# Performance work log

Measured on AMD Instinct MI355X. Metric: run time of the kernel, lower is better.

The kernel has to match this reference:

```python
import jax, jax.numpy as jnp
import numpy as np

N = 50000   # nodes
E = 800000  # edges (avg degree 16)
C = 128     # hidden_channels
G = 128     # graphs in batch
L0, L1 = 512, 256  # linear_hidden_channels
P = 2       # num_params (output per graph)


def setup_inputs() -> dict:
    key = jax.random.key(0)
    ks = iter(jax.random.split(key, 48))

    def w(shape):
        return jax.random.normal(next(ks), shape, jnp.float32) / np.float32(np.sqrt(shape[0]))

    inp = {}
    inp["x"] = jax.random.normal(next(ks), (N, 4), jnp.float32)
    inp["edge_index"] = jax.random.randint(next(ks), (2, E), 0, N, dtype=jnp.int32)
    inp["edge_attr"] = jax.random.normal(next(ks), (E, 3), jnp.float32)
    inp["batch"] = jnp.sort(jax.random.randint(next(ks), (N,), 0, G, dtype=jnp.int32))
    # TransformerConv params: layer 0 (in=4) and shared layer (in=C, applied twice
    # because `[GConv(...)]*(n-1)` reuses the same module object).
    for i, din in enumerate([4, C]):
        inp[f"Wq{i}"] = w((din, C)); inp[f"bq{i}"] = jnp.zeros((C,), jnp.float32)
        inp[f"Wk{i}"] = w((din, C)); inp[f"bk{i}"] = jnp.zeros((C,), jnp.float32)
        inp[f"Wv{i}"] = w((din, C)); inp[f"bv{i}"] = jnp.zeros((C,), jnp.float32)
        inp[f"We{i}"] = w((3, C))   # lin_edge has no bias
        inp[f"Ws{i}"] = w((din, C)); inp[f"bs{i}"] = jnp.zeros((C,), jnp.float32)
    inp["Wl0"] = w((C, L0));  inp["bl0"] = jnp.zeros((L0,), jnp.float32)
    inp["Wl1"] = w((L0, L1)); inp["bl1"] = jnp.zeros((L1,), jnp.float32)
    inp["Wl2"] = w((L1, P));  inp["bl2"] = jnp.zeros((P,), jnp.float32)
    return inp


def tconv(x, src, dst, e_attr, Wq, bq, Wk, bk, Wv, bv, We, Ws, bs):
    # TransformerConv (heads=1, edge_dim, root_weight=True, beta=False)
    n = x.shape[0]
    c = Wq.shape[1]
    q = x @ Wq + bq            # [N, C]
    k = x @ Wk + bk
    v = x @ Wv + bv
    e = e_attr @ We            # [E, C]
    kj = k[src] + e            # [E, C] key at source + edge emb
    vj = v[src] + e            # [E, C] value at source + edge emb
    logits = jnp.sum(q[dst] * kj, axis=-1) / jnp.sqrt(jnp.float32(c))  # [E]
    # softmax over incoming edges of each target node
    m = jax.ops.segment_max(logits, dst, num_segments=n)
    a = jnp.exp(logits - m[dst])
    denom = jax.ops.segment_sum(a, dst, num_segments=n)
    alpha = a / denom[dst]
    out = jax.ops.segment_sum(vj * alpha[:, None], dst, num_segments=n)
    return out + x @ Ws + bs   # root/skip connection


def reference(x, edge_index, edge_attr, batch,
              Wq0, bq0, Wk0, bk0, Wv0, bv0, We0, Ws0, bs0,
              Wq1, bq1, Wk1, bk1, Wv1, bv1, We1, Ws1, bs1,
              Wl0, bl0, Wl1, bl1, Wl2, bl2):
    src, dst = edge_index[0], edge_index[1]
    # layer 0
    h = tconv(x, src, dst, edge_attr, Wq0, bq0, Wk0, bk0, Wv0, bv0, We0, Ws0, bs0)
    h = jax.nn.leaky_relu(h, 0.01)  # dropout is identity in eval
    # layers 1..2 share weights (Python list-multiplication of modules)
    for _ in range(2):
        h = tconv(h, src, dst, edge_attr, Wq1, bq1, Wk1, bk1, Wv1, bv1, We1, Ws1, bs1)
        h = jax.nn.leaky_relu(h, 0.01)
    # global_add_pool
    g = jax.ops.segment_sum(h, batch, num_segments=G)  # [G, C]
    # MLP head
    g = jax.nn.relu(g @ Wl0 + bl0)
    g = jax.nn.relu(g @ Wl1 + bl1)
    g = g @ Wl2 + bl2                                  # [G, 2]
    return jnp.ravel(g)                                # [G*2]
```

## Files before the change

### kernel.cpp

```cpp
#include <hip/hip_runtime.h>
#include <math.h>

#define N_NODES 50000
#define N_EDGES 800000
#define CDIM    128
#define GDIM    128
#define L0DIM   512
#define L1DIM   256

typedef unsigned int uint;
typedef unsigned short ushort;
typedef __attribute__((ext_vector_type(8))) short short8;
typedef __attribute__((ext_vector_type(4))) float f32x4;

__device__ inline ushort f2bf(float f) {
  uint u = __float_as_uint(f);
  uint r = (u + 0x7fffu + ((u >> 16) & 1u)) >> 16;
  return (ushort)r;
}
__device__ inline float bflo(uint u) { return __uint_as_float(u << 16); }
__device__ inline float bfhi(uint u) { return __uint_as_float(u & 0xffff0000u); }

__global__ void hist_kernel(const int* __restrict__ dst, int* counts, int E) {
  int e = blockIdx.x * 256 + threadIdx.x;
  if (e < E) atomicAdd(&counts[dst[e]], 1);
}

__global__ void scan_blocks(const int* __restrict__ counts, int* excl, int* bsums, int N) {
  __shared__ int s[1024];
  int tid = threadIdx.x;
  int i = blockIdx.x * 1024 + tid;
  int v = (i < N) ? counts[i] : 0;
  s[tid] = v;
  __syncthreads();
  for (int off = 1; off < 1024; off <<= 1) {
    int t = (tid >= off) ? s[tid - off] : 0;
    __syncthreads();
    s[tid] += t;
    __syncthreads();
  }
  if (i < N) excl[i] = s[tid] - v;
  if (tid == 1023) bsums[blockIdx.x] = s[1023];
}

__global__ void scan_sums(int* bsums, int nb) {
  int lane = threadIdx.x;
  int orig = (lane < nb) ? bsums[lane] : 0;
  int v = orig;
#pragma unroll
  for (int off = 1; off < 64; off <<= 1) {
    int t = __shfl_up(v, off);
    if (lane >= off) v += t;
  }
  if (lane < nb) bsums[lane] = v - orig;
}

__global__ void scan_add(const int* __restrict__ excl, const int* __restrict__ bsums,
                         int* indptr, int N, int E) {
  int i = blockIdx.x * 1024 + threadIdx.x;
  if (i < N) indptr[i] = excl[i] + bsums[blockIdx.x];
  if (i == 0) indptr[N] = E;
}

__global__ void scatter2_kernel(const int* __restrict__ dst, const int* __restrict__ src,
                                const float* __restrict__ attr,
                                const int* __restrict__ indptr,
                                int* cursor, int* csr_src, float4* csr_attr, int E) {
  int e = blockIdx.x * 256 + threadIdx.x;
  if (e < E) {
    int d = dst[e];
    int pos = atomicAdd(&cursor[d], 1);
    int i = indptr[d] + pos;
    csr_src[i] = src[e];
    csr_attr[i] = make_float4(attr[e * 3 + 0], attr[e * 3 + 1], attr[e * 3 + 2], 0.f);
  }
}

__global__ void l0_qkvs(const float* __restrict__ x,
                        const float* __restrict__ Wq, const float* __restrict__ bq,
                        const float* __restrict__ Wk, const float* __restrict__ bk,
                        const float* __restrict__ Wv, const float* __restrict__ bv,
                        const float* __restrict__ Ws, const float* __restrict__ bs,
                        float* __restrict__ q, ushort* __restrict__ kvb,
                        float* __restrict__ hs, int N) {
  __shared__ float W[4][4][128];
  __shared__ float B[4][128];
  int tid = threadIdx.x;
  for (int i = tid; i < 4 * 128; i += 256) {
    W[0][i >> 7][i & 127] = Wq[i];
    W[1][i >> 7][i & 127] = Wk[i];
    W[2][i >> 7][i & 127] = Wv[i];
    W[3][i >> 7][i & 127] = Ws[i];
  }
  for (int i = tid; i < 128; i += 256) {
    B[0][i] = bq[i]; B[1][i] = bk[i]; B[2][i] = bv[i]; B[3][i] = bs[i];
  }
  __syncthreads();
  int gid = blockIdx.x * 256 + tid;
  int n = gid >> 7, c = gid & 127;
  if (n >= N) return;
  float x0 = x[n * 4 + 0], x1 = x[n * 4 + 1], x2 = x[n * 4 + 2], x3 = x[n * 4 + 3];
  float qv = x0 * W[0][0][c] + x1 * W[0][1][c] + x2 * W[0][2][c] + x3 * W[0][3][c] + B[0][c];
  float kv = x0 * W[1][0][c] + x1 * W[1][1][c] + x2 * W[1][2][c] + x3 * W[1][3][c] + B[1][c];
  float vv = x0 * W[2][0][c] + x1 * W[2][1][c] + x2 * W[2][2][c] + x3 * W[2][3][c] + B[2][c];
  float sv = x0 * W[3][0][c] + x1 * W[3][1][c] + x2 * W[3][2][c] + x3 * W[3][3][c] + B[3][c];
  q[n * 128 + c] = qv;
  kvb[(size_t)n * 256 + c]       = f2bf(kv);
  kvb[(size_t)n * 256 + 128 + c] = f2bf(vv);
  hs[n * 128 + c] = sv;
}

__global__ void prep_w(const float* __restrict__ Wq, const float* __restrict__ Wk,
                       const float* __restrict__ Wv, const float* __restrict__ Ws,
                       ushort* __restrict__ wt) {
  int idx = blockIdx.x * 256 + threadIdx.x;
  int z = idx >> 14, rem = idx & 16383;
  int k_ = rem >> 7, c_ = rem & 127;
  const float* W = (z == 0) ? Wq : (z == 1) ? Wk : (z == 2) ? Wv : Ws;
  wt[z * 16384 + c_ * 128 + k_] = f2bf(W[k_ * 128 + c_]);
}

#define LDA 136
#define TPB_TILES 4
__global__ __launch_bounds__(256) void gemm_mfma(
    const ushort* __restrict__ Hbf, const ushort* __restrict__ wtg,
    const float* __restrict__ bq, const float* __restrict__ bk,
    const float* __restrict__ bv, const float* __restrict__ bs,
    float* __restrict__ q, ushort* __restrict__ kvb,
    float* __restrict__ hs, int N, int nTiles) {
  int z = blockIdx.z;
  const float* bb = (z == 0) ? bq : (z == 1) ? bk : (z == 2) ? bv : bs;
  __shared__ ushort Alds[64 * LDA];
  __shared__ ushort Wlds[128 * LDA];
  int tid = threadIdx.x;

  {
    const uint* wg = (const uint*)(wtg + z * 16384);
    uint* wl = (uint*)Wlds;
    for (int i = tid; i < 8192; i += 256) {
      int c_ = i >> 6, kp = i & 63;
      wl[c_ * (LDA / 2) + kp] = wg[i];
    }
  }

  int w = tid >> 6, lane = tid & 63;
  int m_ = lane & 15, quad = lane >> 4;
  const uint* hg = (const uint*)Hbf;

  for (int tt = 0; tt < TPB_TILES; tt++) {
    int tile = blockIdx.x * TPB_TILES + tt;
    if (tile >= nTiles) break;
    int n0 = tile * 64;
    __syncthreads();
    {
      uint* al = (uint*)Alds;
      for (int i = tid; i < 4096; i += 256) {
        int r = i >> 6, kp = i & 63;
        int grow = n0 + r; grow = (grow < N) ? grow : (N - 1);
        al[r * (LDA / 2) + kp] = hg[(size_t)grow * 64 + kp];
      }
    }
    __syncthreads();

    f32x4 acc[8];
#pragma unroll
    for (int ct = 0; ct < 8; ct++) acc[ct] = 0.f;
#pragma unroll
    for (int kc = 0; kc < 4; kc++) {
      short8 af = *(const short8*)&Alds[(w * 16 + m_) * LDA + kc * 32 + quad * 8];
#pragma unroll
      for (int ct = 0; ct < 8; ct++) {
        short8 bf = *(const short8*)&Wlds[(ct * 16 + m_) * LDA + kc * 32 + quad * 8];
        acc[ct] = __builtin_amdgcn_mfma_f32_16x16x32_bf16(af, bf, acc[ct], 0, 0, 0);
      }
    }

#pragma unroll
    for (int ct = 0; ct < 8; ct++) {
      int col = ct * 16 + m_;
      float bcol = bb[col];
#pragma unroll
      for (int reg = 0; reg < 4; reg++) {
        int n = n0 + w * 16 + quad * 4 + reg;
        if (n < N) {
          float o = acc[ct][reg] + bcol;
          if (z == 0)      q[(size_t)n * 128 + col] = o;
          else if (z == 3) hs[(size_t)n * 128 + col] = o;
          else             kvb[(size_t)n * 256 + ((z == 2) ? 128 : 0) + col] = f2bf(o);
        }
      }
    }
  }
}

__global__ __launch_bounds__(256) void attn_fused(
    const float* __restrict__ q, const ushort* __restrict__ kv,
    const int* __restrict__ indptr, const int* __restrict__ csr_src,
    const float4* __restrict__ csr_attr, const float* __restrict__ We,
    float* __restrict__ h, ushort* __restrict__ hbf, int N) {
  __shared__ float WeS[384];
  int tid = threadIdx.x;
  for (int i = tid; i < 384; i += 256) WeS[i] = We[i];
  __syncthreads();
  int lane = tid & 63;
  int g = lane >> 4, gl = lane & 15;
  int c = gl * 8;
  float we0[8], we1[8], we2[8];
#pragma unroll
  for (int j = 0; j < 8; j++) {
    we0[j] = WeS[c + j]; we1[j] = WeS[128 + c + j]; we2[j] = WeS[256 + c + j];
  }
  const uint* kvw = (const uint*)kv;

  int waveId = blockIdx.x * 4 + (tid >> 6);
  int stride = gridDim.x * 4;

  for (int n = waveId; n < N; n += stride) {
    float4 qa  = *(const float4*)&q[(size_t)n * 128 + c];
    float4 qb4 = *(const float4*)&q[(size_t)n * 128 + c + 4];
    float qv[8] = {qa.x, qa.y, qa.z, qa.w, qb4.x, qb4.y, qb4.z, qb4.w};

    float t0 = 0.f, t1 = 0.f, t2 = 0.f;
#pragma unroll
    for (int j = 0; j < 8; j++) {
      t0 = fmaf(we0[j], qv[j], t0);
      t1 = fmaf(we1[j], qv[j], t1);
      t2 = fmaf(we2[j], qv[j], t2);
    }
#pragma unroll
    for (int off = 1; off < 16; off <<= 1) {
      t0 += __shfl_xor(t0, off);
      t1 += __shfl_xor(t1, off);
      t2 += __shfl_xor(t2, off);
    }

    float4 sk0 = *(const float4*)&h[(size_t)n * 128 + c];
    float4 sk1 = *(const float4*)&h[(size_t)n * 128 + c + 4];
    int beg = indptr[n], end = indptr[n + 1];

    if (end > beg) {
      float m = -3.4e38f, d = 0.f;
      float sa0 = 0.f, sa1 = 0.f, sa2 = 0.f;
      float acc[8];
#pragma unroll
      for (int j = 0; j < 8; j++) acc[j] = 0.f;

      int i = beg + g;
      int sj = 0; float4 at = make_float4(0.f, 0.f, 0.f, 0.f);
      if (i < end) { sj = csr_src[i]; at = csr_attr[i]; }
      for (; i < end; i += 4) {
        int sjc = sj; float4 atc = at;
        int inx = i + 4;
        if (inx < end) { sj = csr_src[inx]; at = csr_attr[inx]; }
        const uint4* kp = (const uint4*)(kvw + (size_t)sjc * 128);
        uint4 kr = kp[gl];
        uint4 vr = kp[16 + gl];
        float kx[8], vx[8];
        kx[0] = bflo(kr.x); kx[1] = bfhi(kr.x); kx[2] = bflo(kr.y); kx[3] = bfhi(kr.y);
        kx[4] = bflo(kr.z); kx[5] = bfhi(kr.z); kx[6] = bflo(kr.w); kx[7] = bfhi(kr.w);
        vx[0] = bflo(vr.x); vx[1] = bfhi(vr.x); vx[2] = bflo(vr.y); vx[3] = bfhi(vr.y);
        vx[4] = bflo(vr.z); vx[5] = bfhi(vr.z); vx[6] = bflo(vr.w); vx[7] = bfhi(vr.w);
        float p = 0.f;
#pragma unroll
        for (int j = 0; j < 8; j++) p = fmaf(qv[j], kx[j], p);
        p += __shfl_xor(p, 1); p += __shfl_xor(p, 2);
        p += __shfl_xor(p, 4); p += __shfl_xor(p, 8);
        p = fmaf(atc.x, t0, p);
        p = fmaf(atc.y, t1, p);
        p = fmaf(atc.z, t2, p);
        float l = p * 0.08838834764831845f;
        float nm = fmaxf(m, l);
        float sf = __expf(m - nm);
        float a = __expf(l - nm);
        d = d * sf + a;
        sa0 = sa0 * sf + a * atc.x;
        sa1 = sa1 * sf + a * atc.y;
        sa2 = sa2 * sf + a * atc.z;
#pragma unroll
        for (int j = 0; j < 8; j++) acc[j] = fmaf(acc[j], sf, a * vx[j]);
        m = nm;
      }
#pragma unroll
      for (int off = 16; off < 64; off <<= 1) {
        float m2 = __shfl_xor(m, off);
        float d2 = __shfl_xor(d, off);
        float nm = fmaxf(m, m2);
        float s1 = __expf(m - nm), s2 = __expf(m2 - nm);
        d = d * s1 + d2 * s2;
        sa0 = sa0 * s1 + __shfl_xor(sa0, off) * s2;
        sa1 = sa1 * s1 + __shfl_xor(sa1, off) * s2;
        sa2 = sa2 * s1 + __shfl_xor(sa2, off) * s2;
#pragma unroll
        for (int j = 0; j < 8; j++) {
          float a2 = __shfl_xor(acc[j], off);
          acc[j] = acc[j] * s1 + a2 * s2;
        }
        m = nm;
      }
      float inv = 1.f / d;
#pragma unroll
      for (int j = 0; j < 8; j++) {
        float ecorr = sa0 * we0[j] + sa1 * we1[j] + sa2 * we2[j];
        float o = (acc[j] + ecorr) * inv;
        if (j < 4) { (&sk0.x)[j] += o; } else { (&sk1.x)[j - 4] += o; }
      }
    }
    sk0.x = (sk0.x > 0.f) ? sk0.x : 0.01f * sk0.x;
    sk0.y = (sk0.y > 0.f) ? sk0.y : 0.01f * sk0.y;
    sk0.z = (sk0.z > 0.f) ? sk0.z : 0.01f * sk0.z;
    sk0.w = (sk0.w > 0.f) ? sk0.w : 0.01f * sk0.w;
    sk1.x = (sk1.x > 0.f) ? sk1.x : 0.01f * sk1.x;
    sk1.y = (sk1.y > 0.f) ? sk1.y : 0.01f * sk1.y;
    sk1.z = (sk1.z > 0.f) ? sk1.z : 0.01f * sk1.z;
    sk1.w = (sk1.w > 0.f) ? sk1.w : 0.01f * sk1.w;
    if (g == 0) {
      *(float4*)&h[(size_t)n * 128 + c] = sk0;
      *(float4*)&h[(size_t)n * 128 + c + 4] = sk1;
      uint4 pb;
      pb.x = (uint)f2bf(sk0.x) | ((uint)f2bf(sk0.y) << 16);
      pb.y = (uint)f2bf(sk0.z) | ((uint)f2bf(sk0.w) << 16);
      pb.z = (uint)f2bf(sk1.x) | ((uint)f2bf(sk1.y) << 16);
      pb.w = (uint)f2bf(sk1.z) | ((uint)f2bf(sk1.w) << 16);
      *(uint4*)&hbf[(size_t)n * 128 + c] = pb;
    }
  }
}

__global__ void pool_kernel(const float* __restrict__ h, const int* __restrict__ batch,
                            float* __restrict__ gout, int N) {
  int tid = threadIdx.x;
  int sub = tid >> 6;
  int c = 2 * (tid & 63);
  int n0 = blockIdx.x * 64 + sub * 16;
  if (n0 >= N) return;
  int n1 = min(n0 + 16, N);
  float a0 = 0.f, a1 = 0.f;
  int cur = batch[n0];
  for (int n = n0; n < n1; n++) {
    int b = batch[n];
    if (b != cur) {
      atomicAdd(&gout[cur * 128 + c], a0);
      atomicAdd(&gout[cur * 128 + c + 1], a1);
      a0 = 0.f; a1 = 0.f; cur = b;
    }
    float2 hv = *(const float2*)&h[(size_t)n * 128 + c];
    a0 += hv.x; a1 += hv.y;
  }
  atomicAdd(&gout[cur * 128 + c], a0);
  atomicAdd(&gout[cur * 128 + c + 1], a1);
}

__global__ __launch_bounds__(256) void mlp_fused(
    const float* __restrict__ gp,
    const float* __restrict__ Wl0, const float* __restrict__ bl0,
    const float* __restrict__ Wl1, const float* __restrict__ bl1,
    const float* __restrict__ Wl2, const float* __restrict__ bl2,
    float* __restrict__ out) {
  int g = blockIdx.x;
  int tid = threadIdx.x;
  __shared__ float xin[CDIM];
  __shared__ float h1[L0DIM];
  __shared__ float h2[L1DIM];
  __shared__ float r0s[4], r1s[4];
  if (tid < CDIM) xin[tid] = gp[g * CDIM + tid];
  __syncthreads();
  for (int c = tid; c < L0DIM; c += 256) {
    float a0 = 0.f, a1 = 0.f, a2 = 0.f, a3 = 0.f;
#pragma unroll 4
    for (int kk = 0; kk < CDIM; kk += 4) {
      a0 = fmaf(xin[kk + 0], Wl0[(kk + 0) * L0DIM + c], a0);
      a1 = fmaf(xin[kk + 1], Wl0[(kk + 1) * L0DIM + c], a1);
      a2 = fmaf(xin[kk + 2], Wl0[(kk + 2) * L0DIM + c], a2);
      a3 = fmaf(xin[kk + 3], Wl0[(kk + 3) * L0DIM + c], a3);
    }
    h1[c] = fmaxf((a0 + a1) + (a2 + a3) + bl0[c], 0.f);
  }
  __syncthreads();
  {
    int c = tid;
    float a0 = 0.f, a1 = 0.f, a2 = 0.f, a3 = 0.f;
#pragma unroll 4
    for (int kk = 0; kk < L0DIM; kk += 4) {
      a0 = fmaf(h1[kk + 0], Wl1[(kk + 0) * L1DIM + c], a0);
      a1 = fmaf(h1[kk + 1], Wl1[(kk + 1) * L1DIM + c], a1);
      a2 = fmaf(h1[kk + 2], Wl1[(kk + 2) * L1DIM + c], a2);
      a3 = fmaf(h1[kk + 3], Wl1[(kk + 3) * L1DIM + c], a3);
    }
    h2[c] = fmaxf((a0 + a1) + (a2 + a3) + bl1[c], 0.f);
  }
  __syncthreads();
  float p0 = h2[tid] * Wl2[tid * 2 + 0];
  float p1 = h2[tid] * Wl2[tid * 2 + 1];
#pragma unroll
  for (int off = 32; off > 0; off >>= 1) {
    p0 += __shfl_down(p0, off);
    p1 += __shfl_down(p1, off);
  }
  int wv = tid >> 6, ln = tid & 63;
  if (ln == 0) { r0s[wv] = p0; r1s[wv] = p1; }
  __syncthreads();
  if (tid == 0) out[g * 2 + 0] = r0s[0] + r0s[1] + r0s[2] + r0s[3] + bl2[0];
  if (tid == 1) out[g * 2 + 1] = r1s[0] + r1s[1] + r1s[2] + r1s[3] + bl2[1];
}

extern "C" void kernel_launch(void* const* d_in, const int* in_sizes, int n_in,
                              void* d_out, int out_size, void* d_ws, size_t ws_size,
                              hipStream_t stream) {
  const int N = N_NODES, E = N_EDGES;
  const float* x    = (const float*)d_in[0];
  const int*   ei   = (const int*)d_in[1];
  const float* attr = (const float*)d_in[2];
  const int*   batch= (const int*)d_in[3];
  const int* src = ei;
  const int* dst = ei + E;

  const float *Wq0 = (const float*)d_in[4],  *bq0 = (const float*)d_in[5];
  const float *Wk0 = (const float*)d_in[6],  *bk0 = (const float*)d_in[7];
  const float *Wv0 = (const float*)d_in[8],  *bv0 = (const float*)d_in[9];
  const float *We0 = (const float*)d_in[10];
  const float *Ws0 = (const float*)d_in[11], *bs0 = (const float*)d_in[12];
  const float *Wq1 = (const float*)d_in[13], *bq1 = (const float*)d_in[14];
  const float *Wk1 = (const float*)d_in[15], *bk1 = (const float*)d_in[16];
  const float *Wv1 = (const float*)d_in[17], *bv1 = (const float*)d_in[18];
  const float *We1 = (const float*)d_in[19];
  const float *Ws1 = (const float*)d_in[20], *bs1 = (const float*)d_in[21];
  const float *Wl0 = (const float*)d_in[22], *bl0 = (const float*)d_in[23];
  const float *Wl1 = (const float*)d_in[24], *bl1 = (const float*)d_in[25];
  const float *Wl2 = (const float*)d_in[26], *bl2 = (const float*)d_in[27];

  size_t off = 0;
  auto carve = [&](size_t bytes) {
    void* p = (char*)d_ws + off;
    off += (bytes + 255) & ~(size_t)255;
    return p;
  };
  float*  hA       = (float*)carve((size_t)N * CDIM * 4);
  float*  hB       = (float*)carve((size_t)N * CDIM * 4);
  float*  qb       = (float*)carve((size_t)N * CDIM * 4);
  ushort* kvb      = (ushort*)carve((size_t)N * 256 * 2);
  ushort* hbf      = (ushort*)carve((size_t)N * CDIM * 2);
  int*    indptr   = (int*)carve((size_t)(N + 1) * 4);
  int*    csr_src  = (int*)carve((size_t)E * 4);
  float4* csr_attr = (float4*)carve((size_t)E * 16);
  int*    cc       = (int*)carve((size_t)2 * N * 4);
  int*    counts   = cc;
  int*    cursor   = cc + N;
  int*    excl     = (int*)carve((size_t)N * 4);
  int*    bsums    = (int*)carve((size_t)64 * 4);
  ushort* wt1      = (ushort*)carve((size_t)4 * 16384 * 2);
  float*  gp       = (float*)carve((size_t)GDIM * CDIM * 4);

  hipMemsetAsync(cc, 0, (size_t)2 * N * 4, stream);
  hipMemsetAsync(gp, 0, (size_t)GDIM * CDIM * 4, stream);

  int nscan = (N + 1023) / 1024;
  hist_kernel<<<(E + 255) / 256, 256, 0, stream>>>(dst, counts, E);
  scan_blocks<<<nscan, 1024, 0, stream>>>(counts, excl, bsums, N);
  scan_sums<<<1, 64, 0, stream>>>(bsums, nscan);
  scan_add<<<nscan, 1024, 0, stream>>>(excl, bsums, indptr, N, E);
  scatter2_kernel<<<(E + 255) / 256, 256, 0, stream>>>(dst, src, attr, indptr, cursor,
                                                       csr_src, csr_attr, E);
  prep_w<<<256, 256, 0, stream>>>(Wq1, Wk1, Wv1, Ws1, wt1);

  int nTiles = (N + 63) / 64;
  dim3 gemmGrid((nTiles + TPB_TILES - 1) / TPB_TILES, 1, 4);
  int attnBlocks = 2048;

  l0_qkvs<<<(N * 128 + 255) / 256, 256, 0, stream>>>(
      x, Wq0, bq0, Wk0, bk0, Wv0, bv0, Ws0, bs0, qb, kvb, hA, N);
  attn_fused<<<attnBlocks, 256, 0, stream>>>(qb, kvb, indptr, csr_src, csr_attr, We0,
                                             hA, hbf, N);

  gemm_mfma<<<gemmGrid, 256, 0, stream>>>(hbf, wt1, bq1, bk1, bv1, bs1, qb, kvb, hB, N, nTiles);
  attn_fused<<<attnBlocks, 256, 0, stream>>>(qb, kvb, indptr, csr_src, csr_attr, We1,
                                             hB, hbf, N);

  gemm_mfma<<<gemmGrid, 256, 0, stream>>>(hbf, wt1, bq1, bk1, bv1, bs1, qb, kvb, hA, N, nTiles);
  attn_fused<<<attnBlocks, 256, 0, stream>>>(qb, kvb, indptr, csr_src, csr_attr, We1,
                                             hA, hbf, N);

  pool_kernel<<<(N + 63) / 64, 256, 0, stream>>>(hA, batch, gp, N);
  mlp_fused<<<GDIM, 256, 0, stream>>>(gp, Wl0, bl0, Wl1, bl1, Wl2, bl2, (float*)d_out);
}
```

Before: 620.0 us.

## Store q in bf16, launch one wave per node, fuse pooling into final attention

```diff
diff --git a/kernel.cpp b/kernel.cpp
--- a/kernel.cpp
+++ b/kernel.cpp
@@ -81,7 +81,7 @@
                         const float* __restrict__ Wk, const float* __restrict__ bk,
                         const float* __restrict__ Wv, const float* __restrict__ bv,
                         const float* __restrict__ Ws, const float* __restrict__ bs,
-                        float* __restrict__ q, ushort* __restrict__ kvb,
+                        ushort* __restrict__ qbf, ushort* __restrict__ kvb,
                         float* __restrict__ hs, int N) {
   __shared__ float W[4][4][128];
   __shared__ float B[4][128];
@@ -104,7 +104,7 @@
   float kv = x0 * W[1][0][c] + x1 * W[1][1][c] + x2 * W[1][2][c] + x3 * W[1][3][c] + B[1][c];
   float vv = x0 * W[2][0][c] + x1 * W[2][1][c] + x2 * W[2][2][c] + x3 * W[2][3][c] + B[2][c];
   float sv = x0 * W[3][0][c] + x1 * W[3][1][c] + x2 * W[3][2][c] + x3 * W[3][3][c] + B[3][c];
-  q[n * 128 + c] = qv;
+  qbf[(size_t)n * 128 + c] = f2bf(qv);
   kvb[(size_t)n * 256 + c]       = f2bf(kv);
   kvb[(size_t)n * 256 + 128 + c] = f2bf(vv);
   hs[n * 128 + c] = sv;
@@ -126,7 +126,7 @@
     const ushort* __restrict__ Hbf, const ushort* __restrict__ wtg,
     const float* __restrict__ bq, const float* __restrict__ bk,
     const float* __restrict__ bv, const float* __restrict__ bs,
-    float* __restrict__ q, ushort* __restrict__ kvb,
+    ushort* __restrict__ qbf, ushort* __restrict__ kvb,
     float* __restrict__ hs, int N, int nTiles) {
   int z = blockIdx.z;
   const float* bb = (z == 0) ? bq : (z == 1) ? bk : (z == 2) ? bv : bs;
@@ -184,7 +184,7 @@
         int n = n0 + w * 16 + quad * 4 + reg;
         if (n < N) {
           float o = acc[ct][reg] + bcol;
-          if (z == 0)      q[(size_t)n * 128 + col] = o;
+          if (z == 0)      qbf[(size_t)n * 128 + col] = f2bf(o);
           else if (z == 3) hs[(size_t)n * 128 + col] = o;
           else             kvb[(size_t)n * 256 + ((z == 2) ? 128 : 0) + col] = f2bf(o);
         }
@@ -193,16 +193,20 @@
   }
 }
 
-__global__ __launch_bounds__(256) void attn_fused(
-    const float* __restrict__ q, const ushort* __restrict__ kv,
+template <int MODE>
+__global__ __launch_bounds__(256) void attn_fused_t(
+    const ushort* __restrict__ qbf, const ushort* __restrict__ kv,
     const int* __restrict__ indptr, const int* __restrict__ csr_src,
     const float4* __restrict__ csr_attr, const float* __restrict__ We,
-    float* __restrict__ h, ushort* __restrict__ hbf, int N) {
+    float* __restrict__ h, ushort* __restrict__ hbf,
+    const int* __restrict__ batch, float* __restrict__ gp, int N) {
   __shared__ float WeS[384];
   int tid = threadIdx.x;
   for (int i = tid; i < 384; i += 256) WeS[i] = We[i];
   __syncthreads();
   int lane = tid & 63;
+  int n = blockIdx.x * 4 + (tid >> 6);
+  if (n >= N) return;
   int g = lane >> 4, gl = lane & 15;
   int c = gl * 8;
   float we0[8], we1[8], we2[8];
@@ -212,107 +216,105 @@
   }
   const uint* kvw = (const uint*)kv;
 
-  int waveId = blockIdx.x * 4 + (tid >> 6);
-  int stride = gridDim.x * 4;
-
-  for (int n = waveId; n < N; n += stride) {
-    float4 qa  = *(const float4*)&q[(size_t)n * 128 + c];
-    float4 qb4 = *(const float4*)&q[(size_t)n * 128 + c + 4];
-    float qv[8] = {qa.x, qa.y, qa.z, qa.w, qb4.x, qb4.y, qb4.z, qb4.w};
-
-    float t0 = 0.f, t1 = 0.f, t2 = 0.f;
+  uint4 qr = ((const uint4*)(qbf + (size_t)n * 128))[gl];
+  float qv[8];
+  qv[0] = bflo(qr.x); qv[1] = bfhi(qr.x); qv[2] = bflo(qr.y); qv[3] = bfhi(qr.y);
+  qv[4] = bflo(qr.z); qv[5] = bfhi(qr.z); qv[6] = bflo(qr.w); qv[7] = bfhi(qr.w);
+
+  float t0 = 0.f, t1 = 0.f, t2 = 0.f;
+#pragma unroll
+  for (int j = 0; j < 8; j++) {
+    t0 = fmaf(we0[j], qv[j], t0);
+    t1 = fmaf(we1[j], qv[j], t1);
+    t2 = fmaf(we2[j], qv[j], t2);
+  }
+#pragma unroll
+  for (int off = 1; off < 16; off <<= 1) {
+    t0 += __shfl_xor(t0, off);
+    t1 += __shfl_xor(t1, off);
+    t2 += __shfl_xor(t2, off);
+  }
+
+  float4 sk0 = *(const float4*)&h[(size_t)n * 128 + c];
+  float4 sk1 = *(const float4*)&h[(size_t)n * 128 + c + 4];
+  int beg = indptr[n], end = indptr[n + 1];
+
+  if (end > beg) {
+    float m = -3.4e38f, d = 0.f;
+    float sa0 = 0.f, sa1 = 0.f, sa2 = 0.f;
+    float acc[8];
+#pragma unroll
+    for (int j = 0; j < 8; j++) acc[j] = 0.f;
+
+    int i = beg + g;
+    int sj = 0; float4 at = make_float4(0.f, 0.f, 0.f, 0.f);
+    if (i < end) { sj = csr_src[i]; at = csr_attr[i]; }
+    for (; i < end; i += 4) {
+      int sjc = sj; float4 atc = at;
+      int inx = i + 4;
+      if (inx < end) { sj = csr_src[inx]; at = csr_attr[inx]; }
+      const uint4* kp = (const uint4*)(kvw + (size_t)sjc * 128);
+      uint4 kr = kp[gl];
+      uint4 vr = kp[16 + gl];
+      float kx[8], vx[8];
+      kx[0] = bflo(kr.x); kx[1] = bfhi(kr.x); kx[2] = bflo(kr.y); kx[3] = bfhi(kr.y);
+      kx[4] = bflo(kr.z); kx[5] = bfhi(kr.z); kx[6] = bflo(kr.w); kx[7] = bfhi(kr.w);
+      vx[0] = bflo(vr.x); vx[1] = bfhi(vr.x); vx[2] = bflo(vr.y); vx[3] = bfhi(vr.y);
+      vx[4] = bflo(vr.z); vx[5] = bfhi(vr.z); vx[6] = bflo(vr.w); vx[7] = bfhi(vr.w);
+      float p = 0.f;
+#pragma unroll
+      for (int j = 0; j < 8; j++) p = fmaf(qv[j], kx[j], p);
+      p += __shfl_xor(p, 1); p += __shfl_xor(p, 2);
+      p += __shfl_xor(p, 4); p += __shfl_xor(p, 8);
+      p = fmaf(atc.x, t0, p);
+      p = fmaf(atc.y, t1, p);
+      p = fmaf(atc.z, t2, p);
+      float l = p * 0.08838834764831845f;
+      float nm = fmaxf(m, l);
+      float sf = __expf(m - nm);
+      float a = __expf(l - nm);
+      d = d * sf + a;
+      sa0 = sa0 * sf + a * atc.x;
+      sa1 = sa1 * sf + a * atc.y;
+      sa2 = sa2 * sf + a * atc.z;
+#pragma unroll
+      for (int j = 0; j < 8; j++) acc[j] = fmaf(acc[j], sf, a * vx[j]);
+      m = nm;
+    }
+#pragma unroll
+    for (int off = 16; off < 64; off <<= 1) {
+      float m2 = __shfl_xor(m, off);
+      float d2 = __shfl_xor(d, off);
+      float nm = fmaxf(m, m2);
+      float s1 = __expf(m - nm), s2 = __expf(m2 - nm);
+      d = d * s1 + d2 * s2;
+      sa0 = sa0 * s1 + __shfl_xor(sa0, off) * s2;
+      sa1 = sa1 * s1 + __shfl_xor(sa1, off) * s2;
+      sa2 = sa2 * s1 + __shfl_xor(sa2, off) * s2;
+#pragma unroll
+      for (int j = 0; j < 8; j++) {
+        float a2 = __shfl_xor(acc[j], off);
+        acc[j] = acc[j] * s1 + a2 * s2;
+      }
+      m = nm;
+    }
+    float inv = 1.f / d;
 #pragma unroll
     for (int j = 0; j < 8; j++) {
-      t0 = fmaf(we0[j], qv[j], t0);
-      t1 = fmaf(we1[j], qv[j], t1);
-      t2 = fmaf(we2[j], qv[j], t2);
-    }
-#pragma unroll
-    for (int off = 1; off < 16; off <<= 1) {
-      t0 += __shfl_xor(t0, off);
-      t1 += __shfl_xor(t1, off);
-      t2 += __shfl_xor(t2, off);
-    }
-
-    float4 sk0 = *(const float4*)&h[(size_t)n * 128 + c];
-    float4 sk1 = *(const float4*)&h[(size_t)n * 128 + c + 4];
-    int beg = indptr[n], end = indptr[n + 1];
-
-    if (end > beg) {
-      float m = -3.4e38f, d = 0.f;
-      float sa0 = 0.f, sa1 = 0.f, sa2 = 0.f;
-      float acc[8];
-#pragma unroll
-      for (int j = 0; j < 8; j++) acc[j] = 0.f;
-
-      int i = beg + g;
-      int sj = 0; float4 at = make_float4(0.f, 0.f, 0.f, 0.f);
-      if (i < end) { sj = csr_src[i]; at = csr_attr[i]; }
-      for (; i < end; i += 4) {
-        int sjc = sj; float4 atc = at;
-        int inx = i + 4;
-        if (inx < end) { sj = csr_src[inx]; at = csr_attr[inx]; }
-        const uint4* kp = (const uint4*)(kvw + (size_t)sjc * 128);
-        uint4 kr = kp[gl];
-        uint4 vr = kp[16 + gl];
-        float kx[8], vx[8];
-        kx[0] = bflo(kr.x); kx[1] = bfhi(kr.x); kx[2] = bflo(kr.y); kx[3] = bfhi(kr.y);
-        kx[4] = bflo(kr.z); kx[5] = bfhi(kr.z); kx[6] = bflo(kr.w); kx[7] = bfhi(kr.w);
-        vx[0] = bflo(vr.x); vx[1] = bfhi(vr.x); vx[2] = bflo(vr.y); vx[3] = bfhi(vr.y);
-        vx[4] = bflo(vr.z); vx[5] = bfhi(vr.z); vx[6] = bflo(vr.w); vx[7] = bfhi(vr.w);
-        float p = 0.f;
-#pragma unroll
-        for (int j = 0; j < 8; j++) p = fmaf(qv[j], kx[j], p);
-        p += __shfl_xor(p, 1); p += __shfl_xor(p, 2);
-        p += __shfl_xor(p, 4); p += __shfl_xor(p, 8);
-        p = fmaf(atc.x, t0, p);
-        p = fmaf(atc.y, t1, p);
-        p = fmaf(atc.z, t2, p);
-        float l = p * 0.08838834764831845f;
-        float nm = fmaxf(m, l);
-        float sf = __expf(m - nm);
-        float a = __expf(l - nm);
-        d = d * sf + a;
-        sa0 = sa0 * sf + a * atc.x;
-        sa1 = sa1 * sf + a * atc.y;
-        sa2 = sa2 * sf + a * atc.z;
-#pragma unroll
-        for (int j = 0; j < 8; j++) acc[j] = fmaf(acc[j], sf, a * vx[j]);
-        m = nm;
-      }
-#pragma unroll
-      for (int off = 16; off < 64; off <<= 1) {
-        float m2 = __shfl_xor(m, off);
-        float d2 = __shfl_xor(d, off);
-        float nm = fmaxf(m, m2);
-        float s1 = __expf(m - nm), s2 = __expf(m2 - nm);
-        d = d * s1 + d2 * s2;
-        sa0 = sa0 * s1 + __shfl_xor(sa0, off) * s2;
-        sa1 = sa1 * s1 + __shfl_xor(sa1, off) * s2;
-        sa2 = sa2 * s1 + __shfl_xor(sa2, off) * s2;
-#pragma unroll
-        for (int j = 0; j < 8; j++) {
-          float a2 = __shfl_xor(acc[j], off);
-          acc[j] = acc[j] * s1 + a2 * s2;
-        }
-        m = nm;
-      }
-      float inv = 1.f / d;
-#pragma unroll
-      for (int j = 0; j < 8; j++) {
-        float ecorr = sa0 * we0[j] + sa1 * we1[j] + sa2 * we2[j];
-        float o = (acc[j] + ecorr) * inv;
-        if (j < 4) { (&sk0.x)[j] += o; } else { (&sk1.x)[j - 4] += o; }
-      }
-    }
-    sk0.x = (sk0.x > 0.f) ? sk0.x : 0.01f * sk0.x;
-    sk0.y = (sk0.y > 0.f) ? sk0.y : 0.01f * sk0.y;
-    sk0.z = (sk0.z > 0.f) ? sk0.z : 0.01f * sk0.z;
-    sk0.w = (sk0.w > 0.f) ? sk0.w : 0.01f * sk0.w;
-    sk1.x = (sk1.x > 0.f) ? sk1.x : 0.01f * sk1.x;
-    sk1.y = (sk1.y > 0.f) ? sk1.y : 0.01f * sk1.y;
-    sk1.z = (sk1.z > 0.f) ? sk1.z : 0.01f * sk1.z;
-    sk1.w = (sk1.w > 0.f) ? sk1.w : 0.01f * sk1.w;
+      float ecorr = sa0 * we0[j] + sa1 * we1[j] + sa2 * we2[j];
+      float o = (acc[j] + ecorr) * inv;
+      if (j < 4) { (&sk0.x)[j] += o; } else { (&sk1.x)[j - 4] += o; }
+    }
+  }
+  sk0.x = (sk0.x > 0.f) ? sk0.x : 0.01f * sk0.x;
+  sk0.y = (sk0.y > 0.f) ? sk0.y : 0.01f * sk0.y;
+  sk0.z = (sk0.z > 0.f) ? sk0.z : 0.01f * sk0.z;
+  sk0.w = (sk0.w > 0.f) ? sk0.w : 0.01f * sk0.w;
+  sk1.x = (sk1.x > 0.f) ? sk1.x : 0.01f * sk1.x;
+  sk1.y = (sk1.y > 0.f) ? sk1.y : 0.01f * sk1.y;
+  sk1.z = (sk1.z > 0.f) ? sk1.z : 0.01f * sk1.z;
+  sk1.w = (sk1.w > 0.f) ? sk1.w : 0.01f * sk1.w;
+  if (MODE == 0) {
     if (g == 0) {
       *(float4*)&h[(size_t)n * 128 + c] = sk0;
       *(float4*)&h[(size_t)n * 128 + c + 4] = sk1;
@@ -323,31 +325,16 @@
       pb.w = (uint)f2bf(sk1.z) | ((uint)f2bf(sk1.w) << 16);
       *(uint4*)&hbf[(size_t)n * 128 + c] = pb;
     }
-  }
-}
-
-__global__ void pool_kernel(const float* __restrict__ h, const int* __restrict__ batch,
-                            float* __restrict__ gout, int N) {
-  int tid = threadIdx.x;
-  int sub = tid >> 6;
-  int c = 2 * (tid & 63);
-  int n0 = blockIdx.x * 64 + sub * 16;
-  if (n0 >= N) return;
-  int n1 = min(n0 + 16, N);
-  float a0 = 0.f, a1 = 0.f;
-  int cur = batch[n0];
-  for (int n = n0; n < n1; n++) {
-    int b = batch[n];
-    if (b != cur) {
-      atomicAdd(&gout[cur * 128 + c], a0);
-      atomicAdd(&gout[cur * 128 + c + 1], a1);
-      a0 = 0.f; a1 = 0.f; cur = b;
-    }
-    float2 hv = *(const float2*)&h[(size_t)n * 128 + c];
-    a0 += hv.x; a1 += hv.y;
-  }
-  atomicAdd(&gout[cur * 128 + c], a0);
-  atomicAdd(&gout[cur * 128 + c + 1], a1);
+  } else {
+    if (g == 0) {
+      int b = batch[n];
+      float* gr = gp + (size_t)b * 128 + c;
+      atomicAdd(&gr[0], sk0.x); atomicAdd(&gr[1], sk0.y);
+      atomicAdd(&gr[2], sk0.z); atomicAdd(&gr[3], sk0.w);
+      atomicAdd(&gr[4], sk1.x); atomicAdd(&gr[5], sk1.y);
+      atomicAdd(&gr[6], sk1.z); atomicAdd(&gr[7], sk1.w);
+    }
+  }
 }
 
 __global__ __launch_bounds__(256) void mlp_fused(
@@ -436,7 +423,7 @@
   };
   float*  hA       = (float*)carve((size_t)N * CDIM * 4);
   float*  hB       = (float*)carve((size_t)N * CDIM * 4);
-  float*  qb       = (float*)carve((size_t)N * CDIM * 4);
+  ushort* qbf      = (ushort*)carve((size_t)N * CDIM * 2);
   ushort* kvb      = (ushort*)carve((size_t)N * 256 * 2);
   ushort* hbf      = (ushort*)carve((size_t)N * CDIM * 2);
   int*    indptr   = (int*)carve((size_t)(N + 1) * 4);
@@ -464,21 +451,20 @@
 
   int nTiles = (N + 63) / 64;
   dim3 gemmGrid((nTiles + TPB_TILES - 1) / TPB_TILES, 1, 4);
-  int attnBlocks = 2048;
+  int naBlocks = (N + 3) / 4;
 
   l0_qkvs<<<(N * 128 + 255) / 256, 256, 0, stream>>>(
-      x, Wq0, bq0, Wk0, bk0, Wv0, bv0, Ws0, bs0, qb, kvb, hA, N);
-  attn_fused<<<attnBlocks, 256, 0, stream>>>(qb, kvb, indptr, csr_src, csr_attr, We0,
-                                             hA, hbf, N);
-
-  gemm_mfma<<<gemmGrid, 256, 0, stream>>>(hbf, wt1, bq1, bk1, bv1, bs1, qb, kvb, hB, N, nTiles);
-  attn_fused<<<attnBlocks, 256, 0, stream>>>(qb, kvb, indptr, csr_src, csr_attr, We1,
-                                             hB, hbf, N);
-
-  gemm_mfma<<<gemmGrid, 256, 0, stream>>>(hbf, wt1, bq1, bk1, bv1, bs1, qb, kvb, hA, N, nTiles);
-  attn_fused<<<attnBlocks, 256, 0, stream>>>(qb, kvb, indptr, csr_src, csr_attr, We1,
-                                             hA, hbf, N);
-
-  pool_kernel<<<(N + 63) / 64, 256, 0, stream>>>(hA, batch, gp, N);
+      x, Wq0, bq0, Wk0, bk0, Wv0, bv0, Ws0, bs0, qbf, kvb, hA, N);
+  attn_fused_t<0><<<naBlocks, 256, 0, stream>>>(qbf, kvb, indptr, csr_src, csr_attr, We0,
+                                                hA, hbf, batch, gp, N);
+
+  gemm_mfma<<<gemmGrid, 256, 0, stream>>>(hbf, wt1, bq1, bk1, bv1, bs1, qbf, kvb, hB, N, nTiles);
+  attn_fused_t<0><<<naBlocks, 256, 0, stream>>>(qbf, kvb, indptr, csr_src, csr_attr, We1,
+                                                hB, hbf, batch, gp, N);
+
+  gemm_mfma<<<gemmGrid, 256, 0, stream>>>(hbf, wt1, bq1, bk1, bv1, bs1, qbf, kvb, hA, N, nTiles);
+  attn_fused_t<1><<<naBlocks, 256, 0, stream>>>(qbf, kvb, indptr, csr_src, csr_attr, We1,
+                                                hA, hbf, batch, gp, N);
+
   mlp_fused<<<GDIM, 256, 0, stream>>>(gp, Wl0, bl0, Wl1, bl1, Wl2, bl2, (float*)d_out);
 }
```

After: 1.035 ms. 1.67x slower.
